# Kernel optimization log

Measured on AMD Instinct MI355X. Metric: run time of the kernel, lower is better.

Reference implementation:

```python
import jax, jax.numpy as jnp
import numpy as np

B, S, H = 4, 2048, 1024
NH, HD = 16, 64  # num heads, head dim

def setup_inputs() -> dict:
    key = jax.random.key(0)
    ks = jax.random.split(key, 4)
    scale = 1.0 / np.sqrt(H)
    return {
        "hidden_states": jax.random.normal(ks[0], (B, S, H), dtype=jnp.float32),
        "attention_mask": jnp.zeros((B, 1, 1, S), dtype=jnp.float32),
        "wq": jax.random.normal(ks[1], (H, H), dtype=jnp.float32) * scale,
        "bq": jnp.zeros((H,), dtype=jnp.float32),
        "wk": jax.random.normal(ks[2], (H, H), dtype=jnp.float32) * scale,
        "bk": jnp.zeros((H,), dtype=jnp.float32),
        "wv": jax.random.normal(ks[3], (H, H), dtype=jnp.float32) * scale,
        "bv": jnp.zeros((H,), dtype=jnp.float32),
    }

def _split_heads(x):
    # [B,S,H] -> [B,NH,S,HD]
    return x.reshape(B, S, NH, HD).transpose(0, 2, 1, 3)

def reference(hidden_states, attention_mask, wq, bq, wk, bk, wv, bv):
    # torch F.linear: x @ W^T + b
    q = _split_heads(hidden_states @ wq.T + bq)
    k = _split_heads(hidden_states @ wk.T + bk)
    v = _split_heads(hidden_states @ wv.T + bv)
    scores = jnp.einsum("bhqd,bhkd->bhqk", q, k) / np.sqrt(HD)
    scores = scores + attention_mask  # additive mask, broadcast [B,1,1,S]
    probs = jax.nn.softmax(scores, axis=-1)  # dropout p=0.0 (eval)
    ctx = jnp.einsum("bhqk,bhkd->bhqd", probs, v)
    # [B,NH,S,HD] -> [B,S,H]
    return ctx.transpose(0, 2, 1, 3).reshape(B, S, H)
```

## Files before the change

### kernel.cpp

```cpp
#include <hip/hip_runtime.h>

typedef unsigned short u16;
typedef unsigned int u32;
typedef __bf16 bf16;
typedef bf16 bf16x8 __attribute__((ext_vector_type(8)));
typedef float f32x4 __attribute__((ext_vector_type(4)));
typedef float f32x16 __attribute__((ext_vector_type(16)));
typedef u16 u16x8 __attribute__((ext_vector_type(8)));
typedef u16 u16x4 __attribute__((ext_vector_type(4)));
typedef u32 u32x4 __attribute__((ext_vector_type(4)));

#define B_ 4
#define S_ 2048
#define H_ 1024
#define NH_ 16
#define HD_ 64
#define M_TOT (B_ * S_)
#define N_TOT (3 * H_)

#if __has_builtin(__builtin_amdgcn_exp2f)
#define EXP2(x) __builtin_amdgcn_exp2f(x)
#else
static __device__ __forceinline__ float exp2_hw(float x) {
    float r; asm("v_exp_f32 %0, %1" : "=v"(r) : "v"(x)); return r;
}
#define EXP2(x) exp2_hw(x)
#endif

__device__ __forceinline__ u16 f2bf(float f) {
    union { float f; unsigned u; } v; v.f = f;
    unsigned r = v.u + 0x7FFFu + ((v.u >> 16) & 1u);
    return (u16)(r >> 16);
}

__device__ __forceinline__ u32 cvt_pk_bf16(float a, float b) {
    u32 r;
    asm("v_cvt_pk_bf16_f32 %0, %1, %2" : "=v"(r) : "v"(a), "v"(b));
    return r;
}
__device__ __forceinline__ void perm32swap(u32& a, u32& b) {
    asm volatile("v_permlane32_swap_b32 %0, %1" : "+v"(a), "+v"(b));
}
__device__ __forceinline__ void gload16(const void* g, void* l) {
    __builtin_amdgcn_global_load_lds(
        (const __attribute__((address_space(1))) void*)g,
        (__attribute__((address_space(3))) void*)l, 16, 0, 0);
}
__device__ __forceinline__ void wait_vm0() {
    asm volatile("s_waitcnt vmcnt(0)" ::: "memory");
}

__global__ __launch_bounds__(256) void cvt_all(
    const float* __restrict__ x, const float* __restrict__ wq,
    const float* __restrict__ wk, const float* __restrict__ wv,
    u16* __restrict__ xb, u16* __restrict__ wb) {
    const int X4 = (M_TOT * H_) / 4;
    const int W4 = (H_ * H_) / 4;
    const int total = X4 + 3 * W4;
    int i = blockIdx.x * blockDim.x + threadIdx.x;
    int stride = gridDim.x * blockDim.x;
    for (; i < total; i += stride) {
        const float* src; u16* dst; int off;
        if (i < X4) { src = x; dst = xb; off = i; }
        else {
            int j = i - X4;
            int w = j >> 18;
            off = j & (W4 - 1);
            src = (w == 0) ? wq : (w == 1) ? wk : wv;
            dst = wb + w * (H_ * H_);
        }
        float4 v = ((const float4*)src)[off];
        u16x4 o = { f2bf(v.x), f2bf(v.y), f2bf(v.z), f2bf(v.w) };
        *(u16x4*)&dst[off * 4] = o;
    }
}

__global__ __launch_bounds__(512, 2) void qkv_gemm(
    const u16* __restrict__ X, const u16* __restrict__ W,
    const float* __restrict__ bq, const float* __restrict__ bk, const float* __restrict__ bv,
    u16* __restrict__ Q, u16* __restrict__ Ko, u16* __restrict__ Vt) {
    __shared__ __align__(16) u16 As[2][256 * 32];
    __shared__ __align__(16) u16 Bs[2][128 * 32];

    const int tid = threadIdx.x;
    const int lane = tid & 63;
    const int wave = tid >> 6;
    const int l31 = lane & 31;
    const int hi = lane >> 5;
    const int m0 = blockIdx.y * 256;
    const int n0 = blockIdx.x * 128;
    const int wr = (wave >> 1) * 64;
    const int wc = (wave & 1) * 64;

    f32x16 acc[2][2];
#pragma unroll
    for (int mf = 0; mf < 2; mf++)
#pragma unroll
        for (int nf = 0; nf < 2; nf++)
#pragma unroll
            for (int i = 0; i < 16; i++) acc[mf][nf][i] = 0.f;

    const int ca = tid;
    const int raA = ca >> 2, caA = (ca & 3) * 8;
    const u16* gA0 = &X[(size_t)(m0 + raA) * H_ + caA];
    const u16* gA1 = &X[(size_t)(m0 + 128 + raA) * H_ + caA];
    const u16* gB0 = &W[(size_t)(n0 + raA) * H_ + caA];
    char* lA = (char*)&As[0][0] + wave * 1024;
    char* lB = (char*)&Bs[0][0] + wave * 1024;

    gload16(gA0, lA);
    gload16(gA1, lA + 8192);
    gload16(gB0, lB);

    for (int k0 = 0; k0 < H_; k0 += 32) {
        const int cur = (k0 >> 5) & 1;
        wait_vm0();
        __builtin_amdgcn_s_barrier();
        if (k0 + 32 < H_) {
            char* dA = lA + (cur ^ 1) * 16384;
            char* dB = lB + (cur ^ 1) * 8192;
            gload16(gA0 + k0 + 32, dA);
            gload16(gA1 + k0 + 32, dA + 8192);
            gload16(gB0 + k0 + 32, dB);
        }
        const u16* Ab = &As[cur][0];
        const u16* Bb = &Bs[cur][0];
        bf16x8 a[2][2], bfr[2][2];
#pragma unroll
        for (int mf = 0; mf < 2; mf++)
#pragma unroll
            for (int ks = 0; ks < 2; ks++)
                a[mf][ks] = *(const bf16x8*)&Ab[(wr + mf * 32 + l31) * 32 + ks * 16 + hi * 8];
#pragma unroll
        for (int nf = 0; nf < 2; nf++)
#pragma unroll
            for (int ks = 0; ks < 2; ks++)
                bfr[nf][ks] = *(const bf16x8*)&Bb[(wc + nf * 32 + l31) * 32 + ks * 16 + hi * 8];
#pragma unroll
        for (int mf = 0; mf < 2; mf++)
#pragma unroll
            for (int nf = 0; nf < 2; nf++)
#pragma unroll
                for (int ks = 0; ks < 2; ks++)
                    acc[mf][nf] = __builtin_amdgcn_mfma_f32_32x32x16_bf16(
                        a[mf][ks], bfr[nf][ks], acc[mf][nf], 0, 0, 0);
    }

    const float QS = 0.125f * 1.44269504f;
    const int which = n0 >> 10;
    const float* bp = (which == 0) ? bq : (which == 1) ? bk : bv;
#pragma unroll
    for (int nf = 0; nf < 2; nf++) {
        int ng = n0 + wc + nf * 32 + l31;
        int nn = ng & 1023;
        float bias = bp[nn];
        int h = nn >> 6, d = nn & 63;
#pragma unroll
        for (int mf = 0; mf < 2; mf++) {
#pragma unroll
            for (int q = 0; q < 4; q++) {
                int mrow0 = m0 + wr + mf * 32 + 8 * q + 4 * hi;
                int bb = mrow0 >> 11, s0 = mrow0 & 2047;
                if (which == 2) {
                    u16x4 pack;
#pragma unroll
                    for (int j = 0; j < 4; j++) pack[j] = f2bf(acc[mf][nf][q * 4 + j] + bias);
                    *(u16x4*)&Vt[((((size_t)bb * NH_ + h) * HD_) + d) * S_ + s0] = pack;
                } else {
                    u16* dst = (which == 0) ? Q : Ko;
                    float scale = (which == 0) ? QS : 1.0f;
#pragma unroll
                    for (int j = 0; j < 4; j++) {
                        float v = (acc[mf][nf][q * 4 + j] + bias) * scale;
                        dst[((((size_t)bb * NH_ + h) * S_) + s0 + j) * HD_ + d] = f2bf(v);
                    }
                }
            }
        }
    }
}

#define KVB 64
#define NT_ (S_ / KVB)

__global__ __launch_bounds__(512, 4) void attn(
    const u16* __restrict__ Q, const u16* __restrict__ K, const u16* __restrict__ Vt,
    const float* __restrict__ mask, float* __restrict__ out) {
    const int head = blockIdx.y;
    const int b = head >> 4, h = head & 15;
    const int q0 = blockIdx.x * 256;
    const int tid = threadIdx.x;
    const int lane = tid & 63;
    const int wave = tid >> 6;
    const int l31 = lane & 31;
    const int hi = lane >> 5;

    const u16* Qh = Q + (size_t)head * S_ * HD_;
    const u16* Kh = K + (size_t)head * S_ * HD_;
    const u16* Vh = Vt + (size_t)head * HD_ * S_;

    __shared__ __align__(16) u16 Kl[2][KVB * HD_];
    __shared__ __align__(16) u16 Vl[2][HD_ * KVB];
    __shared__ int snz;

    if (tid == 0) snz = 0;
    __syncthreads();
    {
        int nz = 0;
        const f32x4* m4 = (const f32x4*)(mask + (size_t)b * S_);
        for (int i = tid; i < S_ / 4; i += 512) {
            f32x4 v = m4[i];
            nz |= (v[0] != 0.f) | (v[1] != 0.f) | (v[2] != 0.f) | (v[3] != 0.f);
        }
        if (__any(nz) && lane == 0) atomicOr(&snz, 1);
    }

    bf16x8 qf[4];
    {
        const u16* qp = &Qh[(size_t)(q0 + wave * 32 + l31) * HD_ + hi * 8];
        qf[0] = *(const bf16x8*)(qp);
        qf[1] = *(const bf16x8*)(qp + 16);
        qf[2] = *(const bf16x8*)(qp + 32);
        qf[3] = *(const bf16x8*)(qp + 48);
    }
    __syncthreads();
    const bool mz = (snz == 0);
    const float* mrow = mask + (size_t)b * S_;
    const float LOG2E = 1.44269504f;

    const int rc = tid >> 3;
    const u32 sc16 = (u32)(((tid & 7) ^ (rc & 7)) * 16);
    const char* kSrc = (const char*)Kh + (size_t)rc * 128 + sc16;
    const char* vSrc = (const char*)Vh + (size_t)rc * (S_ * 2) + sc16;
    char* dK = (char*)&Kl[0][0] + wave * 1024;
    char* dV = (char*)&Vl[0][0] + wave * 1024;

    const u32 swzR = (u32)((l31 & 7) << 4);
    const u32 rowB = (u32)(l31 * 128);

    f32x16 oacc[2];
#pragma unroll
    for (int dh = 0; dh < 2; dh++)
#pragma unroll
        for (int i = 0; i < 16; i++) oacc[dh][i] = 0.f;
    float m = -1e30f, l = 0.f;

    gload16(kSrc, dK);
    gload16(vSrc, dV);

    for (int t = 0; t < NT_; ++t) {
        const int kv0 = t * KVB;
        const int cur = t & 1;
        wait_vm0();
        __builtin_amdgcn_s_barrier();
        if (t + 1 < NT_) {
            gload16(kSrc + (size_t)(kv0 + KVB) * 128, dK + (cur ^ 1) * 8192);
            gload16(vSrc + (size_t)(kv0 + KVB) * 2,   dV + (cur ^ 1) * 8192);
        }
        const char* KB = (const char*)&Kl[cur][0];
        const char* VB = (const char*)&Vl[cur][0];

        f32x16 sc[2];
#pragma unroll
        for (int g = 0; g < 2; g++) {
            f32x16 c;
#pragma unroll
            for (int i = 0; i < 16; i++) c[i] = 0.f;
#pragma unroll
            for (int dk = 0; dk < 4; dk++) {
                bf16x8 kf = *(const bf16x8*)(KB + g * 4096 + rowB +
                                             (((u32)(dk * 32 + hi * 16)) ^ swzR));
                c = __builtin_amdgcn_mfma_f32_32x32x16_bf16(kf, qf[dk], c, 0, 0, 0);
            }
            sc[g] = c;
        }

        if (!mz) {
#pragma unroll
            for (int g = 0; g < 2; g++)
#pragma unroll
                for (int c4 = 0; c4 < 4; c4++) {
                    f32x4 mk = *(const f32x4*)&mrow[kv0 + g * 32 + c4 * 8 + hi * 4];
#pragma unroll
                    for (int e = 0; e < 4; e++) sc[g][c4 * 4 + e] += mk[e] * LOG2E;
                }
        }

        float tm = sc[0][0];
#pragma unroll
        for (int i = 1; i < 16; i++) tm = fmaxf(tm, sc[0][i]);
#pragma unroll
        for (int i = 0; i < 16; i++) tm = fmaxf(tm, sc[1][i]);
        tm = fmaxf(tm, __shfl_xor(tm, 32, 64));
        if (tm > m + 30.f) {
            float fac = EXP2(m - tm);
            l *= fac;
#pragma unroll
            for (int dh = 0; dh < 2; dh++)
#pragma unroll
                for (int i = 0; i < 16; i++) oacc[dh][i] *= fac;
            m = tm;
        }

        float l0 = 0.f, l1 = 0.f, l2 = 0.f, l3 = 0.f;
#pragma unroll
        for (int g = 0; g < 2; g++)
#pragma unroll
            for (int i = 0; i < 16; i += 4) {
                float p0 = EXP2(sc[g][i + 0] - m);
                float p1 = EXP2(sc[g][i + 1] - m);
                float p2 = EXP2(sc[g][i + 2] - m);
                float p3 = EXP2(sc[g][i + 3] - m);
                sc[g][i + 0] = p0; sc[g][i + 1] = p1;
                sc[g][i + 2] = p2; sc[g][i + 3] = p3;
                l0 += p0; l1 += p1; l2 += p2; l3 += p3;
            }
        l += (l0 + l1) + (l2 + l3);

#pragma unroll
        for (int s = 0; s < 4; s++) {
            const int g = s >> 1, r8 = (s & 1) * 8;
            u32 pkA0 = cvt_pk_bf16(sc[g][r8 + 0], sc[g][r8 + 1]);
            u32 pkA1 = cvt_pk_bf16(sc[g][r8 + 2], sc[g][r8 + 3]);
            u32 pkB0 = cvt_pk_bf16(sc[g][r8 + 4], sc[g][r8 + 5]);
            u32 pkB1 = cvt_pk_bf16(sc[g][r8 + 6], sc[g][r8 + 7]);
            perm32swap(pkA0, pkB0);
            perm32swap(pkA1, pkB1);
            union { u32x4 w; bf16x8 v; } pu;
            pu.w = (u32x4){ pkA0, pkA1, pkB0, pkB1 };
            bf16x8 pf = pu.v;
#pragma unroll
            for (int dh = 0; dh < 2; dh++) {
                bf16x8 vf = *(const bf16x8*)(VB + dh * 4096 + rowB +
                                             (((u32)(s * 32 + hi * 16)) ^ swzR));
                oacc[dh] = __builtin_amdgcn_mfma_f32_32x32x16_bf16(vf, pf, oacc[dh], 0, 0, 0);
            }
        }
    }

    float lt = l + __shfl_xor(l, 32, 64);
    float inv = 1.0f / lt;
    const int q = q0 + wave * 32 + l31;
    float* orow = out + ((size_t)b * S_ + q) * H_ + h * HD_;
#pragma unroll
    for (int dh = 0; dh < 2; dh++)
#pragma unroll
        for (int c4 = 0; c4 < 4; c4++) {
            f32x4 v;
#pragma unroll
            for (int e = 0; e < 4; e++) v[e] = oacc[dh][c4 * 4 + e] * inv;
            *(f32x4*)&orow[dh * 32 + c4 * 8 + hi * 4] = v;
        }
}

extern "C" void kernel_launch(void* const* d_in, const int* in_sizes, int n_in,
                              void* d_out, int out_size, void* d_ws, size_t ws_size,
                              hipStream_t stream) {
    const float* hs   = (const float*)d_in[0];
    const float* mask = (const float*)d_in[1];
    const float* wq   = (const float*)d_in[2];
    const float* bq   = (const float*)d_in[3];
    const float* wk   = (const float*)d_in[4];
    const float* bk   = (const float*)d_in[5];
    const float* wv   = (const float*)d_in[6];
    const float* bv   = (const float*)d_in[7];
    float* out = (float*)d_out;

    char* ws = (char*)d_ws;
    u16* Xb = (u16*)ws;
    u16* Wb = (u16*)(ws + 16777216);
    u16* Qb = (u16*)(ws + 23068672);
    u16* Kb = (u16*)(ws + 39845888);
    u16* Vb = (u16*)(ws + 56623104);

    cvt_all<<<2048, 256, 0, stream>>>(hs, wq, wk, wv, Xb, Wb);

    qkv_gemm<<<dim3(N_TOT / 128, M_TOT / 256), 512, 0, stream>>>(
        Xb, Wb, bq, bk, bv, Qb, Kb, Vb);

    attn<<<dim3(S_ / 256, B_ * NH_), 512, 0, stream>>>(Qb, Kb, Vb, mask, out);
}
```

Baseline: 200.3 us.

## Triple-buffer LDS pipelines in QKV GEMM and attention, cache scaled mask in LDS

Both the QKV projection GEMM and the attention kernel move from double to triple buffering, so tile t+2 is prefetched and the wait uses a partial vmcnt instead of draining all loads. The attention kernel also stages the log2e-scaled mask row in LDS, and the Q fragment load is moved earlier. The larger LDS footprint leads attention's launch bound to drop from 4 to 2 blocks per CU, and the GEMM's LDS also grows, which risks lower occupancy.

```diff
diff --git a/kernel.cpp b/kernel.cpp
--- a/kernel.cpp
+++ b/kernel.cpp
@@ -46,9 +46,9 @@
         (const __attribute__((address_space(1))) void*)g,
         (__attribute__((address_space(3))) void*)l, 16, 0, 0);
 }
-__device__ __forceinline__ void wait_vm0() {
-    asm volatile("s_waitcnt vmcnt(0)" ::: "memory");
-}
+__device__ __forceinline__ void wait_vm0() { asm volatile("s_waitcnt vmcnt(0)" ::: "memory"); }
+__device__ __forceinline__ void wait_vm2() { asm volatile("s_waitcnt vmcnt(2)" ::: "memory"); }
+__device__ __forceinline__ void wait_vm3() { asm volatile("s_waitcnt vmcnt(3)" ::: "memory"); }
 
 __global__ __launch_bounds__(256) void cvt_all(
     const float* __restrict__ x, const float* __restrict__ wq,
@@ -75,12 +75,14 @@
     }
 }
 
+#define GNT 32
+
 __global__ __launch_bounds__(512, 2) void qkv_gemm(
     const u16* __restrict__ X, const u16* __restrict__ W,
     const float* __restrict__ bq, const float* __restrict__ bk, const float* __restrict__ bv,
     u16* __restrict__ Q, u16* __restrict__ Ko, u16* __restrict__ Vt) {
-    __shared__ __align__(16) u16 As[2][256 * 32];
-    __shared__ __align__(16) u16 Bs[2][128 * 32];
+    __shared__ __align__(16) u16 As[3][256 * 32];
+    __shared__ __align__(16) u16 Bs[3][128 * 32];
 
     const int tid = threadIdx.x;
     const int lane = tid & 63;
@@ -100,31 +102,32 @@
 #pragma unroll
             for (int i = 0; i < 16; i++) acc[mf][nf][i] = 0.f;
 
-    const int ca = tid;
-    const int raA = ca >> 2, caA = (ca & 3) * 8;
+    const int raA = tid >> 2, caA = (tid & 3) * 8;
     const u16* gA0 = &X[(size_t)(m0 + raA) * H_ + caA];
     const u16* gA1 = &X[(size_t)(m0 + 128 + raA) * H_ + caA];
     const u16* gB0 = &W[(size_t)(n0 + raA) * H_ + caA];
     char* lA = (char*)&As[0][0] + wave * 1024;
     char* lB = (char*)&Bs[0][0] + wave * 1024;
 
-    gload16(gA0, lA);
-    gload16(gA1, lA + 8192);
-    gload16(gB0, lB);
-
-    for (int k0 = 0; k0 < H_; k0 += 32) {
-        const int cur = (k0 >> 5) & 1;
-        wait_vm0();
+    auto stage = [&](int t) {
+        char* dA = lA + (t % 3) * 16384;
+        char* dB = lB + (t % 3) * 8192;
+        gload16(gA0 + t * 32, dA);
+        gload16(gA1 + t * 32, dA + 8192);
+        gload16(gB0 + t * 32, dB);
+    };
+
+    stage(0);
+    stage(1);
+
+    for (int t = 0; t < GNT; ++t) {
+        if (t < GNT - 1) wait_vm3();
+        else             wait_vm0();
         __builtin_amdgcn_s_barrier();
-        if (k0 + 32 < H_) {
-            char* dA = lA + (cur ^ 1) * 16384;
-            char* dB = lB + (cur ^ 1) * 8192;
-            gload16(gA0 + k0 + 32, dA);
-            gload16(gA1 + k0 + 32, dA + 8192);
-            gload16(gB0 + k0 + 32, dB);
-        }
-        const u16* Ab = &As[cur][0];
-        const u16* Bb = &Bs[cur][0];
+        if (t + 2 < GNT) stage(t + 2);
+
+        const u16* Ab = &As[t % 3][0];
+        const u16* Bb = &Bs[t % 3][0];
         bf16x8 a[2][2], bfr[2][2];
 #pragma unroll
         for (int mf = 0; mf < 2; mf++)
@@ -183,7 +186,7 @@
 #define KVB 64
 #define NT_ (S_ / KVB)
 
-__global__ __launch_bounds__(512, 4) void attn(
+__global__ __launch_bounds__(512, 2) void attn(
     const u16* __restrict__ Q, const u16* __restrict__ K, const u16* __restrict__ Vt,
     const float* __restrict__ mask, float* __restrict__ out) {
     const int head = blockIdx.y;
@@ -199,9 +202,19 @@
     const u16* Kh = K + (size_t)head * S_ * HD_;
     const u16* Vh = Vt + (size_t)head * HD_ * S_;
 
-    __shared__ __align__(16) u16 Kl[2][KVB * HD_];
-    __shared__ __align__(16) u16 Vl[2][HD_ * KVB];
+    __shared__ __align__(16) u16 Kl[3][KVB * HD_];
+    __shared__ __align__(16) u16 Vl[3][HD_ * KVB];
+    __shared__ __align__(16) float ml[S_];
     __shared__ int snz;
+
+    bf16x8 qf[4];
+    {
+        const u16* qp = &Qh[(size_t)(q0 + wave * 32 + l31) * HD_ + hi * 8];
+        qf[0] = *(const bf16x8*)(qp);
+        qf[1] = *(const bf16x8*)(qp + 16);
+        qf[2] = *(const bf16x8*)(qp + 32);
+        qf[3] = *(const bf16x8*)(qp + 48);
+    }
 
     if (tid == 0) snz = 0;
     __syncthreads();
@@ -211,22 +224,14 @@
         for (int i = tid; i < S_ / 4; i += 512) {
             f32x4 v = m4[i];
             nz |= (v[0] != 0.f) | (v[1] != 0.f) | (v[2] != 0.f) | (v[3] != 0.f);
+            f32x4 sv = { v[0] * 1.44269504f, v[1] * 1.44269504f,
+                         v[2] * 1.44269504f, v[3] * 1.44269504f };
+            *(f32x4*)&ml[i * 4] = sv;
         }
         if (__any(nz) && lane == 0) atomicOr(&snz, 1);
-    }
-
-    bf16x8 qf[4];
-    {
-        const u16* qp = &Qh[(size_t)(q0 + wave * 32 + l31) * HD_ + hi * 8];
-        qf[0] = *(const bf16x8*)(qp);
-        qf[1] = *(const bf16x8*)(qp + 16);
-        qf[2] = *(const bf16x8*)(qp + 32);
-        qf[3] = *(const bf16x8*)(qp + 48);
     }
     __syncthreads();
     const bool mz = (snz == 0);
-    const float* mrow = mask + (size_t)b * S_;
-    const float LOG2E = 1.44269504f;
 
     const int rc = tid >> 3;
     const u32 sc16 = (u32)(((tid & 7) ^ (rc & 7)) * 16);
@@ -235,6 +240,11 @@
     char* dK = (char*)&Kl[0][0] + wave * 1024;
     char* dV = (char*)&Vl[0][0] + wave * 1024;
 
+    auto stage = [&](int t) {
+        gload16(kSrc + (size_t)t * 8192, dK + (t % 3) * 8192);
+        gload16(vSrc + (size_t)t * 128,  dV + (t % 3) * 8192);
+    };
+
     const u32 swzR = (u32)((l31 & 7) << 4);
     const u32 rowB = (u32)(l31 * 128);
 
@@ -245,20 +255,18 @@
         for (int i = 0; i < 16; i++) oacc[dh][i] = 0.f;
     float m = -1e30f, l = 0.f;
 
-    gload16(kSrc, dK);
-    gload16(vSrc, dV);
+    stage(0);
+    stage(1);
 
     for (int t = 0; t < NT_; ++t) {
         const int kv0 = t * KVB;
-        const int cur = t & 1;
-        wait_vm0();
+        if (t < NT_ - 1) wait_vm2();
+        else             wait_vm0();
         __builtin_amdgcn_s_barrier();
-        if (t + 1 < NT_) {
-            gload16(kSrc + (size_t)(kv0 + KVB) * 128, dK + (cur ^ 1) * 8192);
-            gload16(vSrc + (size_t)(kv0 + KVB) * 2,   dV + (cur ^ 1) * 8192);
-        }
-        const char* KB = (const char*)&Kl[cur][0];
-        const char* VB = (const char*)&Vl[cur][0];
+        if (t + 2 < NT_) stage(t + 2);
+
+        const char* KB = (const char*)&Kl[t % 3][0];
+        const char* VB = (const char*)&Vl[t % 3][0];
 
         f32x16 sc[2];
 #pragma unroll
@@ -280,9 +288,9 @@
             for (int g = 0; g < 2; g++)
 #pragma unroll
                 for (int c4 = 0; c4 < 4; c4++) {
-                    f32x4 mk = *(const f32x4*)&mrow[kv0 + g * 32 + c4 * 8 + hi * 4];
-#pragma unroll
-                    for (int e = 0; e < 4; e++) sc[g][c4 * 4 + e] += mk[e] * LOG2E;
+                    f32x4 mk = *(const f32x4*)&ml[kv0 + g * 32 + c4 * 8 + hi * 4];
+#pragma unroll
+                    for (int e = 0; e < 4; e++) sc[g][c4 * 4 + e] += mk[e];
                 }
         }
 
```

Measured after the change: 207.5 us. 1.04x slower.
